# Optimization experiments

Hardware: AMD Instinct MI355X
Metric: run time of the kernel (lower is better)

Reference implementation:

```python
import jax, jax.numpy as jnp
import numpy as np

NPOINT = 1024
RADIUS = 0.5
NSAMPLE = 32
BN_EPS = 1e-5


def square_distance(src, dst):
    # src: (B,S,3), dst: (B,N,3) -> (B,S,N)
    return (jnp.sum(src ** 2, -1, keepdims=True)
            + jnp.swapaxes(jnp.sum(dst ** 2, -1, keepdims=True), -2, -1)
            - 2.0 * jnp.einsum('bsc,bnc->bsn', src, dst))


def farthest_point_sample(xyz, npoint):
    # xyz: (B,N,3) -> (B,npoint) int32. Deterministic start at index 0.
    B, N, _ = xyz.shape

    def step(carry, _):
        distance, farthest = carry
        centroid = jnp.take_along_axis(xyz, farthest[:, None, None], axis=1)  # (B,1,3)
        d = jnp.sum((xyz - centroid) ** 2, axis=-1)                           # (B,N)
        distance = jnp.minimum(distance, d)
        nxt = jnp.argmax(distance, axis=-1).astype(jnp.int32)
        return (distance, nxt), farthest

    init = (jnp.full((B, N), 1e10, dtype=xyz.dtype), jnp.zeros((B,), jnp.int32))
    _, cents = jax.lax.scan(step, init, None, length=npoint)  # (npoint,B)
    return cents.T


def ball_query(radius, nsample, xyz, new_xyz):
    # -> (B,S,nsample) int32 indices into N; empty slots padded with first hit.
    B, N, _ = xyz.shape
    dist = square_distance(new_xyz, xyz)                       # (B,S,N)
    base = jnp.arange(N, dtype=jnp.int32)[None, None, :]
    idx = jnp.where(dist <= radius ** 2, base, N)
    idx = jnp.sort(idx, axis=-1)[:, :, :nsample]
    first = idx[:, :, :1]
    return jnp.where(idx == N, first, idx)


def index_points(points, idx):
    # points: (B,N,C), idx: (B,...) -> (B,...,C)
    return jax.vmap(lambda p, i: p[i])(points, idx)


def _forward(xyz, features, params):
    # indices are data-dependent but non-differentiable selections
    xyz_c = jax.lax.stop_gradient(xyz)
    fps_idx = farthest_point_sample(xyz_c, NPOINT)             # (B,S)
    group_idx = ball_query(RADIUS, NSAMPLE, xyz_c, index_points(xyz_c, fps_idx))

    new_xyz = index_points(xyz, fps_idx)                       # (B,S,3)
    grouped_xyz = index_points(xyz, group_idx) - new_xyz[:, :, None, :]  # (B,S,K,3)
    grouped = jnp.concatenate([grouped_xyz, index_points(features, group_idx)], -1)  # (B,S,K,Cin)

    for (w, b, g, be) in params:
        # 1x1 Conv2d == per-point linear; BatchNorm2d in training mode:
        # stats over all but channel axis (here axes 0,1,2 of (B,S,K,C)).
        h = jnp.einsum('bskc,dc->bskd', grouped, w) + b
        mean = jnp.mean(h, axis=(0, 1, 2))
        var = jnp.var(h, axis=(0, 1, 2))
        h = (h - mean) * jax.lax.rsqrt(var + BN_EPS) * g + be
        grouped = jax.nn.gelu(h, approximate=False)

    new_features = jnp.max(grouped, axis=2)                    # (B,S,D)
    return new_xyz, new_features


def setup_inputs() -> dict:
    key = jax.random.key(0)
    ks = jax.random.split(key, 16)
    B, N, C = 16, 4096, 64
    inp = {
        'xyz': jax.random.normal(ks[0], (B, N, 3), jnp.float32),
        'features': jax.random.normal(ks[1], (B, N, C), jnp.float32),
    }
    chans = [67, 64, 64, 128]
    for i in range(3):
        cin, cout = chans[i], chans[i + 1]
        inp[f'w{i}'] = jax.random.normal(ks[2 + 4 * i], (cout, cin), jnp.float32) * (1.0 / np.sqrt(cin))
        inp[f'b{i}'] = jnp.zeros((cout,), jnp.float32)
        inp[f'g{i}'] = jnp.ones((cout,), jnp.float32)
        inp[f'be{i}'] = jnp.zeros((cout,), jnp.float32)
    return inp


def reference(xyz, features, w0, b0, g0, be0, w1, b1, g1, be1, w2, b2, g2, be2):
    params = [(w0, b0, g0, be0), (w1, b1, g1, be1), (w2, b2, g2, be2)]
    return _forward(xyz, features, params)
```

## Files before the change

### kernel.cpp

```cpp
#include <hip/hip_runtime.h>

typedef unsigned int uint;
typedef unsigned short ushort;
typedef unsigned long long ull;

#define NB 16
#define NN 4096
#define NS 1024
#define NK 32
#define CIN0 67
#define NPTS (NB*NS*NK)
#define BN_EPS 1e-5f
#define INV_NPTS (1.0f/524288.0f)

#define W0T_OFF 0
#define W1T_OFF 4288
#define W2T_OFF 8384
#define WT_TOTAL 16576

#define FPS_T 256
#define PPT (NN / FPS_T)

#define KMAX_STEP(K, CTRL) do { \
    uint _lo = (uint)(K), _hi = (uint)((K) >> 32); \
    uint _nlo = (uint)__builtin_amdgcn_update_dpp(0, (int)_lo, (CTRL), 0xF, 0xF, true); \
    uint _nhi = (uint)__builtin_amdgcn_update_dpp(0, (int)_hi, (CTRL), 0xF, 0xF, true); \
    ull _nk = ((ull)_nhi << 32) | _nlo; \
    if (_nk > (K)) (K) = _nk; \
  } while (0)

__device__ __forceinline__ void fps_block_merge(
    const uint2* sk, const float4* sc,
    float& cx, float& cy, float& cz, int& fi)
{
  uint4 e01 = *(const uint4*)&sk[0];
  uint4 e23 = *(const uint4*)&sk[2];
  ull k0 = ((ull)e01.y << 32) | e01.x;
  ull k1 = ((ull)e01.w << 32) | e01.z;
  ull k2 = ((ull)e23.y << 32) | e23.x;
  ull k3 = ((ull)e23.w << 32) | e23.z;
  float4 c0 = sc[0], c1 = sc[1], c2 = sc[2], c3 = sc[3];
  ull b = k0; float4 C = c0;
  if (k1 > b) { b = k1; C = c1; }
  if (k2 > b) { b = k2; C = c2; }
  if (k3 > b) { b = k3; C = c3; }
  cx = C.x; cy = C.y; cz = C.z;
  fi = (int)(~(uint)b);
}

__global__ __launch_bounds__(FPS_T) void fps_kernel(
    const float* __restrict__ xyz, float* __restrict__ centers,
    float* __restrict__ out_newxyz)
{
#pragma clang fp contract(off)
  __shared__ float4 sxyz[NN];
  __shared__ int sfar[NS];
  __shared__ __align__(16) uint2  sk[2][FPS_T/64];
  __shared__ __align__(16) float4 sc[2][FPS_T/64];
  const int b = blockIdx.x;
  const int tid = threadIdx.x;
  const int lane = tid & 63;
  const int wv = tid >> 6;
  const float* xb = xyz + (size_t)b * NN * 3;
  for (int i = tid; i < NN; i += FPS_T)
    sxyz[i] = make_float4(xb[i*3+0], xb[i*3+1], xb[i*3+2], 0.f);
  __syncthreads();
  float px[PPT], py[PPT], pz[PPT], dist[PPT];
  const int base = tid * PPT;
#pragma unroll
  for (int j = 0; j < PPT; ++j) {
    float4 P = sxyz[base+j];
    px[j] = P.x; py[j] = P.y; pz[j] = P.z;
    dist[j] = 1e10f;
  }
  float4 C0 = sxyz[0];
  float cx = C0.x, cy = C0.y, cz = C0.z;
  if (tid == 0) sfar[0] = 0;

  for (int it = 1; it < NS; ++it) {
#pragma unroll
    for (int j = 0; j < PPT; ++j) {
      float dx = px[j]-cx, dy = py[j]-cy, dz = pz[j]-cz;
      float d = (dx*dx + dy*dy) + dz*dz;
      float dd = dist[j];
      dist[j] = d < dd ? d : dd;
    }
    float v8[8]; int i8[8];
#pragma unroll
    for (int j = 0; j < 8; ++j) {
      bool t = dist[2*j+1] > dist[2*j];
      v8[j] = t ? dist[2*j+1] : dist[2*j];
      i8[j] = base + (t ? 2*j+1 : 2*j);
    }
    float v4[4]; int i4[4];
#pragma unroll
    for (int j = 0; j < 4; ++j) {
      bool t = v8[2*j+1] > v8[2*j];
      v4[j] = t ? v8[2*j+1] : v8[2*j];
      i4[j] = t ? i8[2*j+1] : i8[2*j];
    }
    float v2[2]; int i2[2];
#pragma unroll
    for (int j = 0; j < 2; ++j) {
      bool t = v4[2*j+1] > v4[2*j];
      v2[j] = t ? v4[2*j+1] : v4[2*j];
      i2[j] = t ? i4[2*j+1] : i4[2*j];
    }
    bool t0 = v2[1] > v2[0];
    float bv = t0 ? v2[1] : v2[0];
    int   bi = t0 ? i2[1] : i2[0];
    ull key = ((ull)__float_as_uint(bv) << 32) | (uint)(~bi);
    KMAX_STEP(key, 0x121);
    KMAX_STEP(key, 0x122);
    KMAX_STEP(key, 0x124);
    KMAX_STEP(key, 0x128);
    KMAX_STEP(key, 0x142);
    KMAX_STEP(key, 0x143);
    const int pb = it & 1;
    if (lane == 63) {
      int iw = (int)(~(uint)key);
      float4 CW = sxyz[iw];
      sk[pb][wv] = make_uint2((uint)key, (uint)(key >> 32));
      sc[pb][wv] = CW;
    }
    __syncthreads();
    int fi;
    fps_block_merge(sk[pb], sc[pb], cx, cy, cz, fi);
    if (tid == 0) sfar[it] = fi;
  }
  __syncthreads();
  for (int s = tid; s < NS; s += FPS_T) {
    int f = sfar[s];
    float4 C = sxyz[f];
    size_t o = ((size_t)b * NS + s) * 3;
    centers[o] = C.x; centers[o+1] = C.y; centers[o+2] = C.z;
    out_newxyz[o] = C.x; out_newxyz[o+1] = C.y; out_newxyz[o+2] = C.z;
  }
}

#define BPAD(i) ((i) + ((i)>>6))
__global__ __launch_bounds__(256,2) void ball_kernel(
    const float* __restrict__ xyz, const float* __restrict__ centers,
    int* __restrict__ group_idx)
{
#pragma clang fp contract(off)
  __shared__ float sx[4160], sy[4160], sz[4160], sq[4160];
  const int bid = blockIdx.x;
  const int b = bid >> 6;
  const int c0 = (bid & 63) << 4;
  const int tid = threadIdx.x;
  const int lane = tid & 63;
  const int wave = tid >> 6;
  const float* xb = xyz + (size_t)b * NN * 3;
  for (int i = tid; i < NN; i += 256) {
    float x = xb[i*3+0], y = xb[i*3+1], z = xb[i*3+2];
    int a = BPAD(i);
    sx[a] = x; sy[a] = y; sz[a] = z;
    sq[a] = (x*x + y*y) + z*z;
  }
  __syncthreads();
  const int a0 = lane * 65;
#pragma unroll 1
  for (int r = 0; r < 4; ++r) {
    const int s = c0 + wave*4 + r;
    const size_t co = ((size_t)b * NS + s) * 3;
    const float cx = centers[co], cy = centers[co+1], cz = centers[co+2];
    const float csq = (cx*cx + cy*cy) + cz*cz;
    unsigned long long mask = 0ull;
#pragma unroll 8
    for (int j = 0; j < 64; ++j) {
      const float dot = (cx*sx[a0+j] + cy*sy[a0+j]) + cz*sz[a0+j];
      const float dist = (csq + sq[a0+j]) - 2.0f*dot;
      mask |= ((unsigned long long)(dist <= 0.25f)) << j;
    }
    int cnt = __popcll(mask);
    int inc = cnt;
#pragma unroll
    for (int m = 1; m < 64; m <<= 1) {
      int o = __shfl_up(inc, m);
      if (lane >= m) inc += o;
    }
    const int pre = inc - cnt;
    const int total = __shfl(inc, 63);
    unsigned long long bal = __ballot(cnt > 0);
    int fl = __ffsll(bal) - 1;
    int myfirst = cnt ? (lane << 6) + __ffsll(mask) - 1 : 0;
    int firstG = __shfl(myfirst, fl);
    int* out = group_idx + ((size_t)b * NS + s) * NK;
    if (pre < NK && cnt) {
      int k = pre;
      unsigned long long m2 = mask;
      while (m2 && k < NK) {
        int j = __ffsll(m2) - 1;
        out[k++] = (lane << 6) + j;
        m2 &= m2 - 1;
      }
    }
    if (total < NK) {
      for (int q2 = total + lane; q2 < NK; q2 += 64) out[q2] = firstG;
    }
  }
}

__global__ __launch_bounds__(256) void prep_kernel(
    const float* __restrict__ w0, const float* __restrict__ w1,
    const float* __restrict__ w2, float* __restrict__ wT)
{
  int i = blockIdx.x*256 + threadIdx.x;
  if (i < 4288) {
    int c = i >> 6, d = i & 63;
    wT[i] = w0[d*CIN0 + c];
  } else if (i < 8384) {
    int j = i - 4288; int c = j >> 6, d = j & 63;
    wT[i] = w1[d*64 + c];
  } else if (i < WT_TOTAL) {
    int j = i - 8384; int c = j >> 7, d = j & 127;
    wT[i] = w2[d*64 + c];
  }
}

__device__ __forceinline__ float gelu_f(float x) {
  float z = fabsf(x) * 0.70710678118654752f;
  float t = __builtin_amdgcn_rcpf(fmaf(0.3275911f, z, 1.0f));
  float p = t * fmaf(t, fmaf(t, fmaf(t, fmaf(t, 1.061405429f, -1.453152027f),
                                     1.421413741f), -0.284496736f), 0.254829592f);
  float ex = __expf(-z*z);
  float er = fmaf(-p, ex, 1.0f);
  float se = __uint_as_float(__float_as_uint(er) | (__float_as_uint(x) & 0x80000000u));
  return 0.5f * x * (1.0f + se);
}
__device__ __forceinline__ float bf_lo(uint u) { return __uint_as_float(u << 16); }
__device__ __forceinline__ float bf_hi(uint u) { return __uint_as_float(u & 0xffff0000u); }
__device__ __forceinline__ uint bfpack(float a, float b) {
  uint ua = __float_as_uint(a), ub = __float_as_uint(b);
  ua = (ua + 0x7fffu + ((ua >> 16) & 1u)) >> 16;
  ub = (ub + 0x7fffu + ((ub >> 16) & 1u)) >> 16;
  return (ua & 0xffffu) | (ub << 16);
}

__device__ __forceinline__ void fmac64(float (&acc)[64], const float* wrow, float xc) {
  const float4* wp = (const float4*)wrow;
#pragma unroll
  for (int i = 0; i < 16; ++i) {
    float4 w = wp[i];
    acc[i*4+0] = fmaf(xc, w.x, acc[i*4+0]);
    acc[i*4+1] = fmaf(xc, w.y, acc[i*4+1]);
    acc[i*4+2] = fmaf(xc, w.z, acc[i*4+2]);
    acc[i*4+3] = fmaf(xc, w.w, acc[i*4+3]);
  }
}
__device__ __forceinline__ void fmac128(float (&acc)[128], const float* wrow, float xc) {
  const float4* wp = (const float4*)wrow;
#pragma unroll
  for (int i = 0; i < 32; ++i) {
    float4 w = wp[i];
    acc[i*4+0] = fmaf(xc, w.x, acc[i*4+0]);
    acc[i*4+1] = fmaf(xc, w.y, acc[i*4+1]);
    acc[i*4+2] = fmaf(xc, w.z, acc[i*4+2]);
    acc[i*4+3] = fmaf(xc, w.w, acc[i*4+3]);
  }
}

__device__ __forceinline__ void layer0(
    const float* __restrict__ xyz, const float* __restrict__ feat,
    const float* __restrict__ centers, const int* __restrict__ gidx,
    const float* wptr, const float* b0v, int p, float (&acc)[64])
{
  const int b = p >> 15;
  const int s = (p & 32767) >> 5;
  const int gi = gidx[p];
#pragma unroll
  for (int d = 0; d < 64; ++d) acc[d] = b0v[d];
  const float* cp = centers + ((size_t)(b*NS + s))*3;
  const float* pp = xyz + ((size_t)(b*NN) + gi)*3;
  const float4* fr = (const float4*)(feat + ((size_t)(b*NN) + gi)*64);
  float4 f = fr[0];
  fmac64(acc, wptr + 0*64, pp[0]-cp[0]);
  fmac64(acc, wptr + 1*64, pp[1]-cp[1]);
  fmac64(acc, wptr + 2*64, pp[2]-cp[2]);
#pragma unroll 1
  for (int q = 0; q < 16; ++q) {
    const int nq = (q < 15) ? q + 1 : 15;
    float4 fn = fr[nq];
    fmac64(acc, wptr + (3+q*4)*64, f.x);
    fmac64(acc, wptr + (4+q*4)*64, f.y);
    fmac64(acc, wptr + (5+q*4)*64, f.z);
    fmac64(acc, wptr + (6+q*4)*64, f.w);
    f = fn;
  }
}

__device__ __forceinline__ void block_colsum64(const float (&v)[64], float* sbuf,
    float* bsum, float* bssq, int cbase)
{
  const int tid = threadIdx.x;
#pragma unroll
  for (int cc = 0; cc < 4; ++cc) {
    __syncthreads();
#pragma unroll
    for (int j = 0; j < 16; ++j) sbuf[tid*17 + j] = v[cc*16 + j];
    __syncthreads();
    const int c = tid & 15, seg = tid >> 4;
    float s = 0.f, q = 0.f;
#pragma unroll
    for (int i = 0; i < 16; ++i) {
      float x = sbuf[(seg*16 + i)*17 + c];
      s += x; q += x*x;
    }
    __syncthreads();
    sbuf[tid*2] = s; sbuf[tid*2+1] = q;
    __syncthreads();
    if (tid < 16) {
      float ss = 0.f, qq = 0.f;
#pragma unroll
      for (int sg = 0; sg < 16; ++sg) {
        ss += sbuf[(sg*16 + tid)*2];
        qq += sbuf[(sg*16 + tid)*2 + 1];
      }
      bsum[cbase + cc*16 + tid] += ss;
      bssq[cbase + cc*16 + tid] += qq;
    }
  }
  __syncthreads();
}

__global__ __launch_bounds__(256,3) void p0_kernel(
    const float* __restrict__ xyz, const float* __restrict__ feat,
    const float* __restrict__ centers, const int* __restrict__ gidx,
    const float* __restrict__ wT, const float* __restrict__ b0,
    ushort* __restrict__ X, float* __restrict__ stat0)
{
  __shared__ float sbuf[4352];
  __shared__ float bsum[64], bssq[64], b0s[64];
  const int tid = threadIdx.x;
  if (tid < 64) { bsum[tid] = 0.f; bssq[tid] = 0.f; b0s[tid] = b0[tid]; }
  __syncthreads();
  const int p = blockIdx.x*256 + tid;
  float acc[64];
  layer0(xyz, feat, centers, gidx, wT + W0T_OFF, b0s, p, acc);
  uint4* xr = (uint4*)(X + (size_t)p*64);
#pragma unroll
  for (int q = 0; q < 8; ++q) {
    uint4 pk;
    pk.x = bfpack(acc[q*8+0], acc[q*8+1]);
    pk.y = bfpack(acc[q*8+2], acc[q*8+3]);
    pk.z = bfpack(acc[q*8+4], acc[q*8+5]);
    pk.w = bfpack(acc[q*8+6], acc[q*8+7]);
    xr[q] = pk;
  }
  block_colsum64(acc, sbuf, bsum, bssq, 0);
  if (tid < 64) {
    atomicAdd(&stat0[tid], bsum[tid]);
    atomicAdd(&stat0[64+tid], bssq[tid]);
  }
}

__global__ __launch_bounds__(256,3) void p1_kernel(
    ushort* X, const float* __restrict__ wT,
    const float* __restrict__ stat0, const float* __restrict__ g0,
    const float* __restrict__ be0, const float* __restrict__ b1,
    float* __restrict__ stat1)
{
  __shared__ float sbuf[4352];
  __shared__ float bsum[64], bssq[64];
  __shared__ float sc[64], sh[64], b1s[64];
  const float* __restrict__ w1g = wT + W1T_OFF;
  const int tid = threadIdx.x;
  if (tid < 64) {
    float m0 = stat0[tid]*INV_NPTS;
    float v0 = stat0[64+tid]*INV_NPTS - m0*m0;
    float s0 = (1.0f/sqrtf(v0 + BN_EPS)) * g0[tid];
    sc[tid] = s0; sh[tid] = be0[tid] - m0*s0;
    b1s[tid] = b1[tid];
    bsum[tid] = 0.f; bssq[tid] = 0.f;
  }
  __syncthreads();
  const int p = blockIdx.x*256 + tid;
  uint4* xr = (uint4*)(X + (size_t)p*64);
  float acc[64];
#pragma unroll
  for (int d = 0; d < 64; ++d) acc[d] = b1s[d];
  uint4 v = xr[0];
#pragma unroll 1
  for (int ch = 0; ch < 8; ++ch) {
    const int nc = (ch < 7) ? ch + 1 : 7;
    uint4 vn = xr[nc];
    const int c = ch*8;
    float x0 = gelu_f(fmaf(bf_lo(v.x), sc[c+0], sh[c+0]));
    float x1 = gelu_f(fmaf(bf_hi(v.x), sc[c+1], sh[c+1]));
    float x2 = gelu_f(fmaf(bf_lo(v.y), sc[c+2], sh[c+2]));
    float x3 = gelu_f(fmaf(bf_hi(v.y), sc[c+3], sh[c+3]));
    float x4 = gelu_f(fmaf(bf_lo(v.z), sc[c+4], sh[c+4]));
    float x5 = gelu_f(fmaf(bf_hi(v.z), sc[c+5], sh[c+5]));
    float x6 = gelu_f(fmaf(bf_lo(v.w), sc[c+6], sh[c+6]));
    float x7 = gelu_f(fmaf(bf_hi(v.w), sc[c+7], sh[c+7]));
    fmac64(acc, w1g + (c+0)*64, x0);
    fmac64(acc, w1g + (c+1)*64, x1);
    fmac64(acc, w1g + (c+2)*64, x2);
    fmac64(acc, w1g + (c+3)*64, x3);
    fmac64(acc, w1g + (c+4)*64, x4);
    fmac64(acc, w1g + (c+5)*64, x5);
    fmac64(acc, w1g + (c+6)*64, x6);
    fmac64(acc, w1g + (c+7)*64, x7);
    v = vn;
  }
#pragma unroll
  for (int q = 0; q < 8; ++q) {
    uint4 pk;
    pk.x = bfpack(acc[q*8+0], acc[q*8+1]);
    pk.y = bfpack(acc[q*8+2], acc[q*8+3]);
    pk.z = bfpack(acc[q*8+4], acc[q*8+5]);
    pk.w = bfpack(acc[q*8+6], acc[q*8+7]);
    xr[q] = pk;
  }
  block_colsum64(acc, sbuf, bsum, bssq, 0);
  if (tid < 64) {
    atomicAdd(&stat1[tid], bsum[tid]);
    atomicAdd(&stat1[64+tid], bssq[tid]);
  }
}

template<bool STORE_H2>
__global__ __launch_bounds__(256,2) void p2_kernel(
    ushort* X, ushort* __restrict__ H2, const float* __restrict__ wT,
    const float* __restrict__ stat1, const float* __restrict__ g1,
    const float* __restrict__ be1, const float* __restrict__ b2,
    float* __restrict__ stat2)
{
  __shared__ float sbuf[4352];
  __shared__ float bsum[128], bssq[128];
  __shared__ float sc[64], sh[64], b2s[128];
  const float* __restrict__ w2g = wT + W2T_OFF;
  const int tid = threadIdx.x;
  if (tid < 64) {
    float m1 = stat1[tid]*INV_NPTS;
    float v1 = stat1[64+tid]*INV_NPTS - m1*m1;
    float s1 = (1.0f/sqrtf(v1 + BN_EPS)) * g1[tid];
    sc[tid] = s1; sh[tid] = be1[tid] - m1*s1;
  }
  if (tid < 128) { b2s[tid] = b2[tid]; bsum[tid] = 0.f; bssq[tid] = 0.f; }
  __syncthreads();
  const int p = blockIdx.x*256 + tid;
  uint4* xr = (uint4*)(X + (size_t)p*64);
  float acc[128];
#pragma unroll
  for (int d = 0; d < 128; ++d) acc[d] = b2s[d];
  uint4 v = xr[0];
#pragma unroll 1
  for (int ch = 0; ch < 8; ++ch) {
    const int nc = (ch < 7) ? ch + 1 : 7;
    uint4 vn = xr[nc];
    const int c = ch*8;
    float x0 = gelu_f(fmaf(bf_lo(v.x), sc[c+0], sh[c+0]));
    float x1 = gelu_f(fmaf(bf_hi(v.x), sc[c+1], sh[c+1]));
    float x2 = gelu_f(fmaf(bf_lo(v.y), sc[c+2], sh[c+2]));
    float x3 = gelu_f(fmaf(bf_hi(v.y), sc[c+3], sh[c+3]));
    float x4 = gelu_f(fmaf(bf_lo(v.z), sc[c+4], sh[c+4]));
    float x5 = gelu_f(fmaf(bf_hi(v.z), sc[c+5], sh[c+5]));
    float x6 = gelu_f(fmaf(bf_lo(v.w), sc[c+6], sh[c+6]));
    float x7 = gelu_f(fmaf(bf_hi(v.w), sc[c+7], sh[c+7]));
    if (!STORE_H2) {
      uint4 pk;
      pk.x = bfpack(x0, x1); pk.y = bfpack(x2, x3);
      pk.z = bfpack(x4, x5); pk.w = bfpack(x6, x7);
      xr[ch] = pk;
    }
    fmac128(acc, w2g + (c+0)*128, x0);
    fmac128(acc, w2g + (c+1)*128, x1);
    fmac128(acc, w2g + (c+2)*128, x2);
    fmac128(acc, w2g + (c+3)*128, x3);
    fmac128(acc, w2g + (c+4)*128, x4);
    fmac128(acc, w2g + (c+5)*128, x5);
    fmac128(acc, w2g + (c+6)*128, x6);
    fmac128(acc, w2g + (c+7)*128, x7);
    v = vn;
  }
  if (STORE_H2) {
    uint4* hr = (uint4*)(H2 + (size_t)p*128);
#pragma unroll
    for (int q = 0; q < 16; ++q) {
      uint4 pk;
      pk.x = bfpack(acc[q*8+0], acc[q*8+1]);
      pk.y = bfpack(acc[q*8+2], acc[q*8+3]);
      pk.z = bfpack(acc[q*8+4], acc[q*8+5]);
      pk.w = bfpack(acc[q*8+6], acc[q*8+7]);
      hr[q] = pk;
    }
  }
#pragma unroll
  for (int half = 0; half < 2; ++half) {
    float tmp[64];
#pragma unroll
    for (int d = 0; d < 64; ++d) tmp[d] = acc[half*64 + d];
    block_colsum64(tmp, sbuf, bsum, bssq, half*64);
  }
  if (tid < 128) {
    atomicAdd(&stat2[tid], bsum[tid]);
    atomicAdd(&stat2[128+tid], bssq[tid]);
  }
}

__global__ __launch_bounds__(128) void fbig_kernel(
    const ushort* __restrict__ H2, const float* __restrict__ stat2,
    const float* __restrict__ g2, const float* __restrict__ be2,
    float* __restrict__ out_feat)
{
  const int d = threadIdx.x;
  const int bs = blockIdx.x;
  const float mean = stat2[d] * INV_NPTS;
  const float var  = stat2[128+d] * INV_NPTS - mean*mean;
  const float scale = (1.0f/sqrtf(var + BN_EPS)) * g2[d];
  const float shift = be2[d] - mean*scale;
  const ushort* rp = H2 + (size_t)bs*NK*128 + d;
  float m = -3.4e38f;
#pragma unroll 4
  for (int k = 0; k < NK; ++k) {
    float t = __uint_as_float(((uint)rp[k*128]) << 16);
    m = fmaxf(m, gelu_f(fmaf(t, scale, shift)));
  }
  out_feat[(size_t)bs*128 + d] = m;
}

__global__ __launch_bounds__(256,2) void fsmall_kernel(
    const ushort* __restrict__ X, const float* __restrict__ wT,
    const float* __restrict__ b2, const float* __restrict__ stat2,
    const float* __restrict__ g2, const float* __restrict__ be2,
    float* __restrict__ out_feat)
{
  __shared__ float b2s[128], sc2[128], sh2[128];
  const float* __restrict__ w2g = wT + W2T_OFF;
  const int tid = threadIdx.x;
  if (tid < 128) {
    b2s[tid] = b2[tid];
    float m2 = stat2[tid]*INV_NPTS;
    float v2 = stat2[128+tid]*INV_NPTS - m2*m2;
    float s2 = (1.0f/sqrtf(v2 + BN_EPS)) * g2[tid];
    sc2[tid] = s2; sh2[tid] = be2[tid] - m2*s2;
  }
  __syncthreads();
  const int p = blockIdx.x*256 + tid;
  const int bs = p >> 5;
  const uint4* xr = (const uint4*)(X + (size_t)p*64);
  float acc[128];
#pragma unroll
  for (int d = 0; d < 128; ++d) acc[d] = b2s[d];
  uint4 v = xr[0];
#pragma unroll 1
  for (int ch = 0; ch < 8; ++ch) {
    const int nc = (ch < 7) ? ch + 1 : 7;
    uint4 vn = xr[nc];
    const int c = ch*8;
    fmac128(acc, w2g + (c+0)*128, bf_lo(v.x));
    fmac128(acc, w2g + (c+1)*128, bf_hi(v.x));
    fmac128(acc, w2g + (c+2)*128, bf_lo(v.y));
    fmac128(acc, w2g + (c+3)*128, bf_hi(v.y));
    fmac128(acc, w2g + (c+4)*128, bf_lo(v.z));
    fmac128(acc, w2g + (c+5)*128, bf_hi(v.z));
    fmac128(acc, w2g + (c+6)*128, bf_lo(v.w));
    fmac128(acc, w2g + (c+7)*128, bf_hi(v.w));
    v = vn;
  }
#pragma unroll
  for (int d = 0; d < 128; ++d) {
    float y = gelu_f(fmaf(acc[d], sc2[d], sh2[d]));
#pragma unroll
    for (int m = 1; m < 32; m <<= 1) y = fmaxf(y, __shfl_xor(y, m));
    acc[d] = y;
  }
  if ((tid & 31) == 0) {
    float4* op = (float4*)(out_feat + (size_t)bs*128);
#pragma unroll
    for (int i = 0; i < 32; ++i)
      op[i] = make_float4(acc[i*4], acc[i*4+1], acc[i*4+2], acc[i*4+3]);
  }
}

__device__ __forceinline__ void chain_to_x2(
    const float* __restrict__ xyz, const float* __restrict__ feat,
    const float* __restrict__ centers, const int* __restrict__ gidx,
    const float* wsh, float* sbuf, const float* prm, int p, float (&x2)[64])
{
  float acc0[64];
  layer0(xyz, feat, centers, gidx, wsh, prm, p, acc0);
#pragma unroll
  for (int c = 0; c < 64; ++c) acc0[c] = gelu_f(fmaf(acc0[c], prm[64+c], prm[128+c]));
#pragma unroll
  for (int d = 0; d < 64; ++d) x2[d] = prm[192+d];
  float* xrow = sbuf + threadIdx.x*17;
#pragma unroll
  for (int cc = 0; cc < 4; ++cc) {
#pragma unroll
    for (int j = 0; j < 16; ++j) xrow[j] = acc0[cc*16 + j];
#pragma unroll 1
    for (int cj = 0; cj < 16; ++cj)
      fmac64(x2, wsh + W1T_OFF + (cc*16+cj)*64, xrow[cj]);
  }
#pragma unroll
  for (int c = 0; c < 64; ++c) x2[c] = gelu_f(fmaf(x2[c], prm[256+c], prm[320+c]));
}

__global__ __launch_bounds__(256,2) void s0_kernel(
    const float* __restrict__ xyz, const float* __restrict__ feat,
    const float* __restrict__ centers, const int* __restrict__ gidx,
    const float* __restrict__ wT, const float* __restrict__ b0,
    float* __restrict__ stat0)
{
  __shared__ float wsh[4288];
  __shared__ float sbuf[4352];
  __shared__ float bsum[64], bssq[64], b0s[64];
  const int tid = threadIdx.x;
  for (int i = tid; i < 1072; i += 256) ((float4*)wsh)[i] = ((const float4*)wT)[i];
  if (tid < 64) { bsum[tid] = 0.f; bssq[tid] = 0.f; b0s[tid] = b0[tid]; }
  __syncthreads();
  const int p = blockIdx.x*256 + tid;
  float acc[64];
  layer0(xyz, feat, centers, gidx, wsh, b0s, p, acc);
  block_colsum64(acc, sbuf, bsum, bssq, 0);
  if (tid < 64) {
    atomicAdd(&stat0[tid], bsum[tid]);
    atomicAdd(&stat0[64+tid], bssq[tid]);
  }
}

__global__ __launch_bounds__(256,2) void s1_kernel(
    const float* __restrict__ xyz, const float* __restrict__ feat,
    const float* __restrict__ centers, const int* __restrict__ gidx,
    const float* __restrict__ wT, const float* __restrict__ stat0,
    const float* __restrict__ g0, const float* __restrict__ be0,
    const float* __restrict__ b0, const float* __restrict__ b1,
    float* __restrict__ stat1)
{
  __shared__ float wsh[8384];
  __shared__ float sbuf[4352];
  __shared__ float bsum[64], bssq[64];
  __shared__ float prm[256];
  const int tid = threadIdx.x;
  for (int i = tid; i < 2096; i += 256) ((float4*)wsh)[i] = ((const float4*)wT)[i];
  if (tid < 64) {
    float m0 = stat0[tid]*INV_NPTS;
    float v0 = stat0[64+tid]*INV_NPTS - m0*m0;
    float sc0 = (1.0f/sqrtf(v0 + BN_EPS)) * g0[tid];
    prm[tid] = b0[tid]; prm[64+tid] = sc0; prm[128+tid] = be0[tid] - m0*sc0;
    prm[192+tid] = b1[tid];
    bsum[tid] = 0.f; bssq[tid] = 0.f;
  }
  __syncthreads();
  const int p = blockIdx.x*256 + tid;
  float acc0[64];
  layer0(xyz, feat, centers, gidx, wsh, prm, p, acc0);
#pragma unroll
  for (int c = 0; c < 64; ++c) acc0[c] = gelu_f(fmaf(acc0[c], prm[64+c], prm[128+c]));
  float acc1[64];
#pragma unroll
  for (int d = 0; d < 64; ++d) acc1[d] = prm[192+d];
  float* xrow = sbuf + tid*17;
#pragma unroll
  for (int cc = 0; cc < 4; ++cc) {
#pragma unroll
    for (int j = 0; j < 16; ++j) xrow[j] = acc0[cc*16 + j];
#pragma unroll 1
    for (int cj = 0; cj < 16; ++cj)
      fmac64(acc1, wsh + W1T_OFF + (cc*16+cj)*64, xrow[cj]);
  }
  block_colsum64(acc1, sbuf, bsum, bssq, 0);
  if (tid < 64) {
    atomicAdd(&stat1[tid], bsum[tid]);
    atomicAdd(&stat1[64+tid], bssq[tid]);
  }
}

__global__ __launch_bounds__(256,2) void s2_kernel(
    const float* __restrict__ xyz, const float* __restrict__ feat,
    const float* __restrict__ centers, const int* __restrict__ gidx,
    const float* __restrict__ wT,
    const float* __restrict__ stat0, const float* __restrict__ g0,
    const float* __restrict__ be0, const float* __restrict__ b0,
    const float* __restrict__ b1, const float* __restrict__ stat1,
    const float* __restrict__ g1, const float* __restrict__ be1,
    const float* __restrict__ b2, float* __restrict__ stat2)
{
  __shared__ float wsh[8384];
  __shared__ float sbuf[4352];
  __shared__ float bsum[128], bssq[128];
  __shared__ float prm[512];
  const int tid = threadIdx.x;
  for (int i = tid; i < 2096; i += 256) ((float4*)wsh)[i] = ((const float4*)wT)[i];
  if (tid < 64) {
    float m0 = stat0[tid]*INV_NPTS;
    float v0 = stat0[64+tid]*INV_NPTS - m0*m0;
    float sc0 = (1.0f/sqrtf(v0 + BN_EPS)) * g0[tid];
    prm[tid] = b0[tid]; prm[64+tid] = sc0; prm[128+tid] = be0[tid] - m0*sc0;
    float m1 = stat1[tid]*INV_NPTS;
    float v1 = stat1[64+tid]*INV_NPTS - m1*m1;
    float sc1 = (1.0f/sqrtf(v1 + BN_EPS)) * g1[tid];
    prm[192+tid] = b1[tid]; prm[256+tid] = sc1; prm[320+tid] = be1[tid] - m1*sc1;
  }
  if (tid < 128) { prm[384+tid] = b2[tid]; bsum[tid] = 0.f; bssq[tid] = 0.f; }
  __syncthreads();
  const int p = blockIdx.x*256 + tid;
  float x2[64];
  chain_to_x2(xyz, feat, centers, gidx, wsh, sbuf, prm, p, x2);
  __syncthreads();
  for (int i = tid; i < 2048; i += 256)
    ((float4*)wsh)[i] = ((const float4*)(wT + W2T_OFF))[i];
  __syncthreads();
  float* xrow = sbuf + tid*17;
#pragma unroll 1
  for (int half = 0; half < 2; ++half) {
    float a2[64];
#pragma unroll
    for (int d = 0; d < 64; ++d) a2[d] = prm[384 + half*64 + d];
#pragma unroll
    for (int cc = 0; cc < 4; ++cc) {
#pragma unroll
      for (int j = 0; j < 16; ++j) xrow[j] = x2[cc*16 + j];
#pragma unroll 1
      for (int cj = 0; cj < 16; ++cj)
        fmac64(a2, wsh + (cc*16+cj)*128 + half*64, xrow[cj]);
    }
    block_colsum64(a2, sbuf, bsum, bssq, half*64);
  }
  if (tid < 128) {
    atomicAdd(&stat2[tid], bsum[tid]);
    atomicAdd(&stat2[128+tid], bssq[tid]);
  }
}

__global__ __launch_bounds__(256,2) void fin_kernel(
    const float* __restrict__ xyz, const float* __restrict__ feat,
    const float* __restrict__ centers, const int* __restrict__ gidx,
    const float* __restrict__ wT,
    const float* __restrict__ stat0, const float* __restrict__ g0,
    const float* __restrict__ be0, const float* __restrict__ b0,
    const float* __restrict__ b1, const float* __restrict__ stat1,
    const float* __restrict__ g1, const float* __restrict__ be1,
    const float* __restrict__ b2, const float* __restrict__ stat2,
    const float* __restrict__ g2, const float* __restrict__ be2,
    float* __restrict__ out_feat)
{
  __shared__ float wsh[8384];
  __shared__ float sbuf[4352];
  __shared__ float prm[768];
  const int tid = threadIdx.x;
  for (int i = tid; i < 2096; i += 256) ((float4*)wsh)[i] = ((const float4*)wT)[i];
  if (tid < 64) {
    float m0 = stat0[tid]*INV_NPTS;
    float v0 = stat0[64+tid]*INV_NPTS - m0*m0;
    float sc0 = (1.0f/sqrtf(v0 + BN_EPS)) * g0[tid];
    prm[tid] = b0[tid]; prm[64+tid] = sc0; prm[128+tid] = be0[tid] - m0*sc0;
    float m1 = stat1[tid]*INV_NPTS;
    float v1 = stat1[64+tid]*INV_NPTS - m1*m1;
    float sc1 = (1.0f/sqrtf(v1 + BN_EPS)) * g1[tid];
    prm[192+tid] = b1[tid]; prm[256+tid] = sc1; prm[320+tid] = be1[tid] - m1*sc1;
  }
  if (tid < 128) {
    prm[384+tid] = b2[tid];
    float m2 = stat2[tid]*INV_NPTS;
    float v2 = stat2[128+tid]*INV_NPTS - m2*m2;
    float sc2 = (1.0f/sqrtf(v2 + BN_EPS)) * g2[tid];
    prm[512+tid] = sc2; prm[640+tid] = be2[tid] - m2*sc2;
  }
  __syncthreads();
  const int p = blockIdx.x*256 + tid;
  const int b = p >> 15;
  const int s = (p & 32767) >> 5;
  float x2[64];
  chain_to_x2(xyz, feat, centers, gidx, wsh, sbuf, prm, p, x2);
  __syncthreads();
  for (int i = tid; i < 2048; i += 256)
    ((float4*)wsh)[i] = ((const float4*)(wT + W2T_OFF))[i];
  __syncthreads();
  float* xrow = sbuf + tid*17;
#pragma unroll 1
  for (int half = 0; half < 2; ++half) {
    float a2[64];
#pragma unroll
    for (int d = 0; d < 64; ++d) a2[d] = prm[384 + half*64 + d];
#pragma unroll
    for (int cc = 0; cc < 4; ++cc) {
#pragma unroll
      for (int j = 0; j < 16; ++j) xrow[j] = x2[cc*16 + j];
#pragma unroll 1
      for (int cj = 0; cj < 16; ++cj)
        fmac64(a2, wsh + (cc*16+cj)*128 + half*64, xrow[cj]);
    }
#pragma unroll
    for (int d = 0; d < 64; ++d) {
      float y = gelu_f(fmaf(a2[d], prm[512 + half*64 + d], prm[640 + half*64 + d]));
#pragma unroll
      for (int m = 1; m < 32; m <<= 1) y = fmaxf(y, __shfl_xor(y, m));
      a2[d] = y;
    }
    if ((tid & 31) == 0) {
      float4* op = (float4*)(out_feat + ((size_t)(b*NS + s))*128 + half*64);
#pragma unroll
      for (int i = 0; i < 16; ++i)
        op[i] = make_float4(a2[i*4], a2[i*4+1], a2[i*4+2], a2[i*4+3]);
    }
  }
}

extern "C" void kernel_launch(void* const* d_in, const int* in_sizes, int n_in,
                              void* d_out, int out_size, void* d_ws, size_t ws_size,
                              hipStream_t stream) {
  (void)in_sizes; (void)n_in; (void)out_size;
  const float* xyz      = (const float*)d_in[0];
  const float* features = (const float*)d_in[1];
  const float* w0  = (const float*)d_in[2];
  const float* b0  = (const float*)d_in[3];
  const float* g0  = (const float*)d_in[4];
  const float* be0 = (const float*)d_in[5];
  const float* w1  = (const float*)d_in[6];
  const float* b1  = (const float*)d_in[7];
  const float* g1  = (const float*)d_in[8];
  const float* be1 = (const float*)d_in[9];
  const float* w2  = (const float*)d_in[10];
  const float* b2  = (const float*)d_in[11];
  const float* g2  = (const float*)d_in[12];
  const float* be2 = (const float*)d_in[13];

  float* out = (float*)d_out;
  float* out_newxyz = out;
  float* out_feat   = out + NB*NS*3;

  char* ws = (char*)d_ws;
  size_t off = 0;
  float* centers   = (float*)(ws + off); off += (size_t)NB*NS*3*4;
  int*   group_idx = (int*)(ws + off);   off += (size_t)NPTS*4;
  float* stats     = (float*)(ws + off); off += 512*4;
  off = (off + 255) & ~(size_t)255;
  float* wT        = (float*)(ws + off); off += (size_t)WT_TOTAL*4;
  off = (off + 255) & ~(size_t)255;
  const size_t base_end = off;
  const size_t X_bytes  = (size_t)NPTS*64*2;
  const size_t H2_bytes = (size_t)NPTS*128*2;
  ushort* X  = (ushort*)(ws + base_end);
  ushort* H2 = (ushort*)(ws + base_end + X_bytes);

  const bool tier_big   = ws_size >= base_end + X_bytes + H2_bytes;
  const bool tier_small = !tier_big && ws_size >= base_end + X_bytes;
  if (ws_size < base_end) return;

  float* stat0 = stats;
  float* stat1 = stats + 128;
  float* stat2 = stats + 256;

  (void)hipMemsetAsync(stats, 0, 2048, stream);
  prep_kernel<<<65, 256, 0, stream>>>(w0, w1, w2, wT);
  fps_kernel<<<NB, FPS_T, 0, stream>>>(xyz, centers, out_newxyz);
  ball_kernel<<<NB*64, 256, 0, stream>>>(xyz, centers, group_idx);

  if (tier_big || tier_small) {
    p0_kernel<<<NPTS/256, 256, 0, stream>>>(xyz, features, centers, group_idx,
                                            wT, b0, X, stat0);
    p1_kernel<<<NPTS/256, 256, 0, stream>>>(X, wT, stat0, g0, be0, b1, stat1);
    if (tier_big) {
      p2_kernel<true><<<NPTS/256, 256, 0, stream>>>(X, H2, wT, stat1, g1, be1, b2, stat2);
      fbig_kernel<<<NB*NS, 128, 0, stream>>>(H2, stat2, g2, be2, out_feat);
    } else {
      p2_kernel<false><<<NPTS/256, 256, 0, stream>>>(X, H2, wT, stat1, g1, be1, b2, stat2);
      fsmall_kernel<<<NPTS/256, 256, 0, stream>>>(X, wT, b2, stat2, g2, be2, out_feat);
    }
  } else {
    s0_kernel<<<NPTS/256, 256, 0, stream>>>(xyz, features, centers, group_idx, wT, b0, stat0);
    s1_kernel<<<NPTS/256, 256, 0, stream>>>(xyz, features, centers, group_idx, wT,
                                            stat0, g0, be0, b0, b1, stat1);
    s2_kernel<<<NPTS/256, 256, 0, stream>>>(xyz, features, centers, group_idx, wT,
                                            stat0, g0, be0, b0, b1, stat1, g1, be1, b2, stat2);
    fin_kernel<<<NPTS/256, 256, 0, stream>>>(xyz, features, centers, group_idx, wT,
                                             stat0, g0, be0, b0, b1, stat1, g1, be1, b2,
                                             stat2, g2, be2, out_feat);
  }
}
```

Before: 1.366 ms.

## Precompute layer-0 feature projection per source point before gathering

Layer 0 is linear, so the feature part (64 input channels) is now projected once per source point (B*N = 65536 rows) into an fp32 buffer F0 with bias folded in. p0 then gathers the 64-wide projected row and adds only the 3 relative-xyz terms, instead of a 67x64 matmul per grouped point (524288 points). This cuts layer-0 FLOPs about 8x, at the cost of an extra kernel and 16MB of workspace writes and gathered reads. It is used only when the workspace is large enough.

```diff
diff --git a/kernel.cpp b/kernel.cpp
--- a/kernel.cpp
+++ b/kernel.cpp
@@ -10,6 +10,7 @@
 #define NK 32
 #define CIN0 67
 #define NPTS (NB*NS*NK)
+#define NROWS (NB*NN)
 #define BN_EPS 1e-5f
 #define INV_NPTS (1.0f/524288.0f)
 
@@ -324,11 +325,40 @@
   __syncthreads();
 }
 
+__global__ __launch_bounds__(256,3) void f0_kernel(
+    const float* __restrict__ feat, const float* __restrict__ wT,
+    const float* __restrict__ b0, float* __restrict__ F0)
+{
+  const int r = blockIdx.x*256 + threadIdx.x;
+  const float* wf = wT + W0T_OFF + 3*64;
+  float acc[64];
+#pragma unroll
+  for (int d = 0; d < 64; ++d) acc[d] = b0[d];
+  const float4* fr = (const float4*)(feat + (size_t)r*64);
+  float4 f = fr[0];
+#pragma unroll 1
+  for (int q = 0; q < 16; ++q) {
+    const int nq = (q < 15) ? q + 1 : 15;
+    float4 fn = fr[nq];
+    fmac64(acc, wf + (q*4+0)*64, f.x);
+    fmac64(acc, wf + (q*4+1)*64, f.y);
+    fmac64(acc, wf + (q*4+2)*64, f.z);
+    fmac64(acc, wf + (q*4+3)*64, f.w);
+    f = fn;
+  }
+  float4* orow = (float4*)(F0 + (size_t)r*64);
+#pragma unroll
+  for (int q = 0; q < 16; ++q)
+    orow[q] = make_float4(acc[q*4], acc[q*4+1], acc[q*4+2], acc[q*4+3]);
+}
+
+template<bool WITH_F0>
 __global__ __launch_bounds__(256,3) void p0_kernel(
     const float* __restrict__ xyz, const float* __restrict__ feat,
     const float* __restrict__ centers, const int* __restrict__ gidx,
     const float* __restrict__ wT, const float* __restrict__ b0,
-    ushort* __restrict__ X, float* __restrict__ stat0)
+    const float* __restrict__ F0, ushort* __restrict__ X,
+    float* __restrict__ stat0)
 {
   __shared__ float sbuf[4352];
   __shared__ float bsum[64], bssq[64], b0s[64];
@@ -337,7 +367,24 @@
   __syncthreads();
   const int p = blockIdx.x*256 + tid;
   float acc[64];
-  layer0(xyz, feat, centers, gidx, wT + W0T_OFF, b0s, p, acc);
+  if constexpr (WITH_F0) {
+    const int b = p >> 15;
+    const int s = (p & 32767) >> 5;
+    const int gi = gidx[p];
+    const float4* f0r = (const float4*)(F0 + ((size_t)(b*NN) + gi)*64);
+#pragma unroll
+    for (int q = 0; q < 16; ++q) {
+      float4 v = f0r[q];
+      acc[q*4+0] = v.x; acc[q*4+1] = v.y; acc[q*4+2] = v.z; acc[q*4+3] = v.w;
+    }
+    const float* cp = centers + ((size_t)(b*NS + s))*3;
+    const float* pp = xyz + ((size_t)(b*NN) + gi)*3;
+    fmac64(acc, wT + W0T_OFF + 0*64, pp[0]-cp[0]);
+    fmac64(acc, wT + W0T_OFF + 1*64, pp[1]-cp[1]);
+    fmac64(acc, wT + W0T_OFF + 2*64, pp[2]-cp[2]);
+  } else {
+    layer0(xyz, feat, centers, gidx, wT + W0T_OFF, b0s, p, acc);
+  }
   uint4* xr = (uint4*)(X + (size_t)p*64);
 #pragma unroll
   for (int q = 0; q < 8; ++q) {
@@ -834,12 +881,17 @@
   const size_t base_end = off;
   const size_t X_bytes  = (size_t)NPTS*64*2;
   const size_t H2_bytes = (size_t)NPTS*128*2;
+  const size_t F0_bytes = (size_t)NROWS*64*4;
   ushort* X  = (ushort*)(ws + base_end);
   ushort* H2 = (ushort*)(ws + base_end + X_bytes);
 
   const bool tier_big   = ws_size >= base_end + X_bytes + H2_bytes;
   const bool tier_small = !tier_big && ws_size >= base_end + X_bytes;
   if (ws_size < base_end) return;
+  const size_t f0_off = tier_big ? base_end + X_bytes + H2_bytes
+                                 : base_end + X_bytes;
+  const bool use_f0 = (tier_big || tier_small) && (ws_size >= f0_off + F0_bytes);
+  float* F0 = (float*)(ws + f0_off);
 
   float* stat0 = stats;
   float* stat1 = stats + 128;
@@ -847,12 +899,18 @@
 
   (void)hipMemsetAsync(stats, 0, 2048, stream);
   prep_kernel<<<65, 256, 0, stream>>>(w0, w1, w2, wT);
+  if (use_f0)
+    f0_kernel<<<NROWS/256, 256, 0, stream>>>(features, wT, b0, F0);
   fps_kernel<<<NB, FPS_T, 0, stream>>>(xyz, centers, out_newxyz);
   ball_kernel<<<NB*64, 256, 0, stream>>>(xyz, centers, group_idx);
 
   if (tier_big || tier_small) {
-    p0_kernel<<<NPTS/256, 256, 0, stream>>>(xyz, features, centers, group_idx,
-                                            wT, b0, X, stat0);
+    if (use_f0)
+      p0_kernel<true><<<NPTS/256, 256, 0, stream>>>(xyz, features, centers, group_idx,
+                                                    wT, b0, F0, X, stat0);
+    else
+      p0_kernel<false><<<NPTS/256, 256, 0, stream>>>(xyz, features, centers, group_idx,
+                                                     wT, b0, F0, X, stat0);
     p1_kernel<<<NPTS/256, 256, 0, stream>>>(X, wT, stat0, g0, be0, b1, stat1);
     if (tier_big) {
       p2_kernel<true><<<NPTS/256, 256, 0, stream>>>(X, H2, wT, stat1, g1, be1, b2, stat2);
```

After: 1.363 ms, median of 2. About the same (-0.2%).
